# Kernel tuning notes

Hardware: AMD Instinct MI355X
Metric: run time of the kernel (lower is better)

## Reference

```python
import jax, jax.numpy as jnp
import numpy as np

N_NODES = 100000
N_EDGES = 600000
D = 128
BN_EPS = 1e-5


def _segment_mean(msgs, seg_ids, num_segments):
    # sum messages per destination node, divide by in-degree (0-deg nodes -> 0)
    s = jax.ops.segment_sum(msgs, seg_ids, num_segments=num_segments)
    cnt = jax.ops.segment_sum(jnp.ones((msgs.shape[0],), msgs.dtype), seg_ids,
                              num_segments=num_segments)
    return s / jnp.maximum(cnt, 1.0)[:, None]


def setup_inputs() -> dict:
    key = jax.random.key(0)
    ks = jax.random.split(key, 8)
    sc = 1.0 / np.sqrt(D)
    return {
        "node_embs": jax.random.normal(ks[0], (N_NODES, D), jnp.float32),
        "edge_embs": jax.random.normal(ks[1], (N_EDGES, D), jnp.float32),
        "W_O": jax.random.normal(ks[2], (D, D), jnp.float32) * sc,
        "b_O": jnp.zeros((D,), jnp.float32),
        "W_I": jax.random.normal(ks[3], (D, D), jnp.float32) * sc,
        "b_I": jnp.zeros((D,), jnp.float32),
        "W_S": jax.random.normal(ks[4], (D, D), jnp.float32) * sc,
        "b_S": jnp.zeros((D,), jnp.float32),
        "gamma": jnp.ones((D,), jnp.float32),
        "beta": jnp.zeros((D,), jnp.float32),
        "src": jax.random.randint(ks[5], (N_EDGES,), 0, N_NODES),
        "dst": jax.random.randint(ks[6], (N_EDGES,), 0, N_NODES),
    }


def reference(node_embs, edge_embs, W_O, b_O, W_I, b_I, W_S, b_S, gamma, beta, src, dst):
    N = node_embs.shape[0]
    # comp_opt == 'TransE': message = u_sub_e = h_src - h_edge
    # original graph: aggregate at dst -> ho
    ho = _segment_mean(node_embs[src] - edge_embs, dst, N)
    # reverse graph: edges flipped, aggregate at original src -> hi
    hi = _segment_mean(node_embs[dst] - edge_embs, src, N)
    # dropout is identity in eval; combine three projections (weights are [out,in])
    h = ((ho @ W_O.T + b_O) + (hi @ W_I.T + b_I) + (node_embs @ W_S.T + b_S)) / 3.0
    # BatchNorm1d with batch statistics (training-mode normalization, biased var)
    mu = jnp.mean(h, axis=0)
    var = jnp.mean((h - mu) ** 2, axis=0)
    h = (h - mu) * jax.lax.rsqrt(var + BN_EPS) * gamma + beta
    return h
```

## Files before the change

kernel.cpp:

```cpp
#include <hip/hip_runtime.h>
#include <hip/hip_bf16.h>

#define NN 100000
#define NE 600000
#define DD 128
#define NBLK 98

typedef __attribute__((ext_vector_type(8))) short short8_t;
typedef __attribute__((ext_vector_type(4))) float float4_t;

__device__ __forceinline__ unsigned short f2bf(float f) {
    union { float f; unsigned int i; } v; v.f = f;
    unsigned int r = v.i + 0x7fffu + ((v.i >> 16) & 1u);
    return (unsigned short)(r >> 16);
}


__global__ __launch_bounds__(256) void k_hist(
    const int* __restrict__ src, const int* __restrict__ dst,
    int* __restrict__ cnt_o, int* __restrict__ cnt_i)
{
    int e = blockIdx.x * 256 + threadIdx.x;
    if (e < NE) {
        atomicAdd(&cnt_o[dst[e]], 1);
        atomicAdd(&cnt_i[src[e]], 1);
    }
}

__global__ __launch_bounds__(256) void k_scanA(
    const int* __restrict__ cnt_o, const int* __restrict__ cnt_i,
    int* __restrict__ ptr_o, int* __restrict__ ptr_i, int* __restrict__ bsum)
{
    __shared__ int sh[256];
    const int* cnt = blockIdx.y ? cnt_i : cnt_o;
    int* ptr       = blockIdx.y ? ptr_i : ptr_o;
    int t = threadIdx.x;
    int base = blockIdx.x * 1024 + t * 4;
    int c[4];
    #pragma unroll
    for (int j = 0; j < 4; j++) c[j] = (base + j < NN) ? cnt[base + j] : 0;
    int s = c[0] + c[1] + c[2] + c[3];
    sh[t] = s;
    __syncthreads();
    for (int off = 1; off < 256; off <<= 1) {
        int v = (t >= off) ? sh[t - off] : 0;
        __syncthreads();
        sh[t] += v;
        __syncthreads();
    }
    int excl = sh[t] - s;
    int e0 = excl, e1 = e0 + c[0], e2 = e1 + c[1], e3 = e2 + c[2];
    if (base     < NN) ptr[base]     = e0;
    if (base + 1 < NN) ptr[base + 1] = e1;
    if (base + 2 < NN) ptr[base + 2] = e2;
    if (base + 3 < NN) ptr[base + 3] = e3;
    if (t == 255) bsum[blockIdx.y * 128 + blockIdx.x] = sh[255];
}

__global__ __launch_bounds__(128) void k_scanB(int* __restrict__ bsum)
{
    __shared__ int sh[128];
    int t = threadIdx.x;
    int* b = bsum + blockIdx.y * 128;
    int v = (t < NBLK) ? b[t] : 0;
    sh[t] = v;
    __syncthreads();
    for (int off = 1; off < 128; off <<= 1) {
        int u = (t >= off) ? sh[t - off] : 0;
        __syncthreads();
        sh[t] += u;
        __syncthreads();
    }
    b[t] = sh[t] - v;
}

__global__ __launch_bounds__(256) void k_scanC(
    int* __restrict__ ptr_o, int* __restrict__ ptr_i, const int* __restrict__ bsum)
{
    int* ptr = blockIdx.y ? ptr_i : ptr_o;
    int off = bsum[blockIdx.y * 128 + blockIdx.x];
    int base = blockIdx.x * 1024 + threadIdx.x * 4;
    #pragma unroll
    for (int j = 0; j < 4; j++)
        if (base + j < NN) ptr[base + j] += off;
    if (blockIdx.x == 0 && threadIdx.x == 0) ptr[NN] = NE;
}

__global__ __launch_bounds__(256) void k_fill(
    const int* __restrict__ src, const int* __restrict__ dst,
    const int* __restrict__ ptr_o, const int* __restrict__ ptr_i,
    int* __restrict__ cur_o, int* __restrict__ cur_i,
    int2* __restrict__ list_o, int2* __restrict__ list_i)
{
    int e = blockIdx.x * 256 + threadIdx.x;
    if (e < NE) {
        int s = src[e], t = dst[e];
        int p = atomicAdd(&cur_o[t], 1);
        list_o[ptr_o[t] + p] = make_int2(e, s);
        int q = atomicAdd(&cur_i[s], 1);
        list_i[ptr_i[s] + q] = make_int2(e, t);
    }
}

__global__ __launch_bounds__(256) void k_gather(
    const float* __restrict__ node, const float* __restrict__ edge,
    const int* __restrict__ ptr_o, const int* __restrict__ ptr_i,
    const int2* __restrict__ list_o, const int2* __restrict__ list_i,
    float* __restrict__ acc_o, float* __restrict__ acc_i)
{
    int gid = blockIdx.x * 4 + (threadIdx.x >> 6);
    int l = threadIdx.x & 63;
    int half = l >> 5;
    int li = l & 31;
    int dirI = gid >= NN;
    int n = gid - (dirI ? NN : 0);
    const int* ptr   = dirI ? ptr_i  : ptr_o;
    const int2* list = dirI ? list_i : list_o;
    float* acc       = dirI ? acc_i  : acc_o;

    int p0 = ptr[n], p1 = ptr[n + 1];
    int deg = p1 - p0;
    int degc = (deg < 64) ? deg : 64;

    int2 eu = make_int2(0, 0);
    if (l < degc) eu = list[p0 + l];

    float4_t a = {0.f, 0.f, 0.f, 0.f};
    for (int t = 0; t < degc; t += 8) {
        int es[4], us[4];
        float ms[4];
        float4_t xs[4], ys[4];
        #pragma unroll
        for (int b = 0; b < 4; b++) {
            int i0 = t + 2 * b;
            int l0 = (i0     < 64) ? i0     : 0;
            int l1 = (i0 + 1 < 64) ? i0 + 1 : 0;
            int e0 = __builtin_amdgcn_readlane(eu.x, l0);
            int u0 = __builtin_amdgcn_readlane(eu.y, l0);
            int e1 = __builtin_amdgcn_readlane(eu.x, l1);
            int u1 = __builtin_amdgcn_readlane(eu.y, l1);
            es[b] = half ? e1 : e0;
            us[b] = half ? u1 : u0;
            ms[b] = (i0 + half < degc) ? 1.0f : 0.0f;
        }
        #pragma unroll
        for (int b = 0; b < 4; b++) {
            xs[b] = *((const float4_t*)(node + (size_t)us[b] * DD) + li);
            ys[b] = *((const float4_t*)(edge + (size_t)es[b] * DD) + li);
        }
        #pragma unroll
        for (int b = 0; b < 4; b++) {
            #pragma unroll
            for (int c = 0; c < 4; c++)
                a[c] = fmaf(xs[b][c] - ys[b][c], ms[b], a[c]);
        }
    }
    for (int j = p0 + 64 + half; j < p1; j += 2) {
        int2 t = list[j];
        float4_t x = *((const float4_t*)(node + (size_t)t.y * DD) + li);
        float4_t y = *((const float4_t*)(edge + (size_t)t.x * DD) + li);
        a += x - y;
    }

    float4_t b;
    #pragma unroll
    for (int c = 0; c < 4; c++) b[c] = __shfl_xor(a[c], 32);
    a += b;

    float inv = (deg > 0) ? 1.0f / (float)deg : 0.0f;
    a *= inv;
    if (half == 0)
        *((float4_t*)(acc + (size_t)n * DD) + li) = a;
}

__global__ __launch_bounds__(256) void k_gemm(
    const float* acc_o, const float* acc_i,
    const float* __restrict__ node,
    const float* __restrict__ W0, const float* __restrict__ W1, const float* __restrict__ W2,
    const float* __restrict__ b0, const float* __restrict__ b1, const float* __restrict__ b2,
    float* h, float* __restrict__ col_sum, float* __restrict__ col_sumsq)
{
    __shared__ unsigned short s_a[32 * 40];
    __shared__ unsigned short s_b[128 * 40];
    __shared__ float s_red[2 * 4 * 128];

    const int tid = threadIdx.x;
    const int n0 = blockIdx.x * 32;
    const int w  = tid >> 6;
    const int l  = tid & 63;
    const int q  = l >> 4;
    const int li = l & 15;

    float4_t acc[2][2];
    #pragma unroll
    for (int i = 0; i < 2; i++)
        #pragma unroll
        for (int j = 0; j < 2; j++) acc[i][j] = (float4_t){0.f, 0.f, 0.f, 0.f};

    const int srow = tid >> 3;
    const int skq  = tid & 7;

    for (int kc = 0; kc < 12; kc++) {
        const int m  = kc >> 2;
        const int k0 = (kc & 3) * 32;
        const float* X = (m == 0) ? acc_o : (m == 1) ? acc_i : node;
        const float* W = (m == 0) ? W0    : (m == 1) ? W1    : W2;

        __syncthreads();

        {
            float4 v = *(const float4*)&X[(size_t)(n0 + srow) * DD + k0 + 4 * skq];
            ushort4 o = { f2bf(v.x), f2bf(v.y), f2bf(v.z), f2bf(v.w) };
            *(ushort4*)&s_a[srow * 40 + 4 * skq] = o;
        }
        #pragma unroll
        for (int p = 0; p < 4; p++) {
            int row = 32 * p + srow;
            float4 v = *(const float4*)&W[row * DD + k0 + 4 * skq];
            ushort4 o = { f2bf(v.x), f2bf(v.y), f2bf(v.z), f2bf(v.w) };
            *(ushort4*)&s_b[row * 40 + 4 * skq] = o;
        }
        __syncthreads();

        short8_t af0 = *(const short8_t*)&s_a[li * 40 + q * 8];
        short8_t af1 = *(const short8_t*)&s_a[(16 + li) * 40 + q * 8];
        short8_t bf0 = *(const short8_t*)&s_b[(32 * w + li) * 40 + q * 8];
        short8_t bf1 = *(const short8_t*)&s_b[(32 * w + 16 + li) * 40 + q * 8];

        acc[0][0] = __builtin_amdgcn_mfma_f32_16x16x32_bf16(af0, bf0, acc[0][0], 0, 0, 0);
        acc[0][1] = __builtin_amdgcn_mfma_f32_16x16x32_bf16(af0, bf1, acc[0][1], 0, 0, 0);
        acc[1][0] = __builtin_amdgcn_mfma_f32_16x16x32_bf16(af1, bf0, acc[1][0], 0, 0, 0);
        acc[1][1] = __builtin_amdgcn_mfma_f32_16x16x32_bf16(af1, bf1, acc[1][1], 0, 0, 0);
    }

    const float third = 1.0f / 3.0f;
    #pragma unroll
    for (int j = 0; j < 2; j++) {
        int c = 32 * w + 16 * j + li;
        float bsum = b0[c] + b1[c] + b2[c];
        float s = 0.f, sq = 0.f;
        #pragma unroll
        for (int i = 0; i < 2; i++)
            #pragma unroll
            for (int reg = 0; reg < 4; reg++) {
                int r = n0 + 16 * i + q * 4 + reg;
                float v = (acc[i][j][reg] + bsum) * third;
                h[(size_t)r * DD + c] = v;
                s += v; sq += v * v;
            }
        s_red[q * 128 + c]       = s;
        s_red[512 + q * 128 + c] = sq;
    }
    __syncthreads();
    if (tid < 128) {
        float s = 0.f, sq = 0.f;
        #pragma unroll
        for (int r4 = 0; r4 < 4; r4++) {
            s  += s_red[r4 * 128 + tid];
            sq += s_red[512 + r4 * 128 + tid];
        }
        unsafeAtomicAdd(col_sum + tid, s);
        unsafeAtomicAdd(col_sumsq + tid, sq);
    }
}

__global__ void k_stats(const float* __restrict__ col_sum, const float* __restrict__ col_sumsq,
                        const float* __restrict__ gamma, const float* __restrict__ beta,
                        float* __restrict__ sc, float* __restrict__ bs)
{
    int t = threadIdx.x;
    float mu  = col_sum[t]   * (1.0f / NN);
    float var = col_sumsq[t] * (1.0f / NN) - mu * mu;
    var = fmaxf(var, 0.0f);
    float rs = rsqrtf(var + 1e-5f);
    float g = gamma[t];
    sc[t] = rs * g;
    bs[t] = beta[t] - mu * rs * g;
}

__global__ __launch_bounds__(256) void k_norm(const float* __restrict__ h,
        const float* __restrict__ sc, const float* __restrict__ bs,
        float* __restrict__ out)
{
    __shared__ float ssc[128], sbs[128];
    int tid = threadIdx.x;
    if (tid < 128) { ssc[tid] = sc[tid]; sbs[tid] = bs[tid]; }
    __syncthreads();
    size_t base = ((size_t)blockIdx.x * 256 + tid) * 4;
    float4 v = *(const float4*)(h + base);
    int j = (int)(base & 127);
    float4 o;
    o.x = fmaf(v.x, ssc[j],     sbs[j]);
    o.y = fmaf(v.y, ssc[j + 1], sbs[j + 1]);
    o.z = fmaf(v.z, ssc[j + 2], sbs[j + 2]);
    o.w = fmaf(v.w, ssc[j + 3], sbs[j + 3]);
    *(float4*)(out + base) = o;
}

extern "C" void kernel_launch(void* const* d_in, const int* in_sizes, int n_in,
                              void* d_out, int out_size, void* d_ws, size_t ws_size,
                              hipStream_t stream)
{
    const float* node  = (const float*)d_in[0];
    const float* edge  = (const float*)d_in[1];
    const float* W0    = (const float*)d_in[2];
    const float* b0    = (const float*)d_in[3];
    const float* W1    = (const float*)d_in[4];
    const float* b1    = (const float*)d_in[5];
    const float* W2    = (const float*)d_in[6];
    const float* b2    = (const float*)d_in[7];
    const float* gamma = (const float*)d_in[8];
    const float* beta  = (const float*)d_in[9];
    const int* src = (const int*)d_in[10];
    const int* dst = (const int*)d_in[11];
    float* out = (float*)d_out;

    const size_t NB = (size_t)NN * DD;
    float* acc_o = (float*)d_ws;
    float* acc_i = acc_o + NB;
    int* cnt_o = (int*)(acc_i + NB);
    int* cnt_i = cnt_o + NN;
    int* cur_o = cnt_i + NN;
    int* cur_i = cur_o + NN;
    float* col_sum   = (float*)(cur_i + NN);
    float* col_sumsq = col_sum + DD;
    int* ptr_o = (int*)(col_sumsq + DD);
    int* ptr_i = ptr_o + (NN + 1);
    int* bsum  = ptr_i + (NN + 1);
    int2* list_o = (int2*)(bsum + 256);
    int2* list_i = list_o + NE;
    float* sc = (float*)(list_i + NE);
    float* bs = sc + DD;
    float* h  = acc_o;

    size_t zbytes = (size_t)(4 * NN + 2 * DD) * sizeof(int);
    hipMemsetAsync(cnt_o, 0, zbytes, stream);

    int egrid = (NE + 255) / 256;
    k_hist <<<egrid, 256, 0, stream>>>(src, dst, cnt_o, cnt_i);
    k_scanA<<<dim3(NBLK, 2), 256, 0, stream>>>(cnt_o, cnt_i, ptr_o, ptr_i, bsum);
    k_scanB<<<dim3(1, 2), 128, 0, stream>>>(bsum);
    k_scanC<<<dim3(NBLK, 2), 256, 0, stream>>>(ptr_o, ptr_i, bsum);
    k_fill <<<egrid, 256, 0, stream>>>(src, dst, ptr_o, ptr_i, cur_o, cur_i, list_o, list_i);
    k_gather<<<(2 * NN) / 4, 256, 0, stream>>>(node, edge,
                                               ptr_o, ptr_i, list_o, list_i, acc_o, acc_i);
    k_gemm<<<NN / 32, 256, 0, stream>>>(acc_o, acc_i, node,
                                        W0, W1, W2, b0, b1, b2,
                                        h, col_sum, col_sumsq);
    k_stats<<<1, 128, 0, stream>>>(col_sum, col_sumsq, gamma, beta, sc, bs);
    k_norm<<<(NN * DD) / 1024, 256, 0, stream>>>(h, sc, bs, out);
}
```

Measured before the change: 827.1 us.

## Fuse neighbor gather into GEMM kernel with bf16 aggregates kept in LDS

After: 759.2 us. -8.2%, faster.

```diff
diff --git a/kernel.cpp b/kernel.cpp
--- a/kernel.cpp
+++ b/kernel.cpp
@@ -102,94 +102,105 @@
     }
 }
 
-__global__ __launch_bounds__(256) void k_gather(
+__global__ __launch_bounds__(256) void k_gg(
     const float* __restrict__ node, const float* __restrict__ edge,
     const int* __restrict__ ptr_o, const int* __restrict__ ptr_i,
     const int2* __restrict__ list_o, const int2* __restrict__ list_i,
-    float* __restrict__ acc_o, float* __restrict__ acc_i)
-{
-    int gid = blockIdx.x * 4 + (threadIdx.x >> 6);
-    int l = threadIdx.x & 63;
-    int half = l >> 5;
-    int li = l & 31;
-    int dirI = gid >= NN;
-    int n = gid - (dirI ? NN : 0);
-    const int* ptr   = dirI ? ptr_i  : ptr_o;
-    const int2* list = dirI ? list_i : list_o;
-    float* acc       = dirI ? acc_i  : acc_o;
-
-    int p0 = ptr[n], p1 = ptr[n + 1];
-    int deg = p1 - p0;
-    int degc = (deg < 64) ? deg : 64;
-
-    int2 eu = make_int2(0, 0);
-    if (l < degc) eu = list[p0 + l];
-
-    float4_t a = {0.f, 0.f, 0.f, 0.f};
-    for (int t = 0; t < degc; t += 8) {
-        int es[4], us[4];
-        float ms[4];
-        float4_t xs[4], ys[4];
-        #pragma unroll
-        for (int b = 0; b < 4; b++) {
-            int i0 = t + 2 * b;
-            int l0 = (i0     < 64) ? i0     : 0;
-            int l1 = (i0 + 1 < 64) ? i0 + 1 : 0;
-            int e0 = __builtin_amdgcn_readlane(eu.x, l0);
-            int u0 = __builtin_amdgcn_readlane(eu.y, l0);
-            int e1 = __builtin_amdgcn_readlane(eu.x, l1);
-            int u1 = __builtin_amdgcn_readlane(eu.y, l1);
-            es[b] = half ? e1 : e0;
-            us[b] = half ? u1 : u0;
-            ms[b] = (i0 + half < degc) ? 1.0f : 0.0f;
-        }
-        #pragma unroll
-        for (int b = 0; b < 4; b++) {
-            xs[b] = *((const float4_t*)(node + (size_t)us[b] * DD) + li);
-            ys[b] = *((const float4_t*)(edge + (size_t)es[b] * DD) + li);
-        }
-        #pragma unroll
-        for (int b = 0; b < 4; b++) {
-            #pragma unroll
-            for (int c = 0; c < 4; c++)
-                a[c] = fmaf(xs[b][c] - ys[b][c], ms[b], a[c]);
-        }
-    }
-    for (int j = p0 + 64 + half; j < p1; j += 2) {
-        int2 t = list[j];
-        float4_t x = *((const float4_t*)(node + (size_t)t.y * DD) + li);
-        float4_t y = *((const float4_t*)(edge + (size_t)t.x * DD) + li);
-        a += x - y;
-    }
-
-    float4_t b;
-    #pragma unroll
-    for (int c = 0; c < 4; c++) b[c] = __shfl_xor(a[c], 32);
-    a += b;
-
-    float inv = (deg > 0) ? 1.0f / (float)deg : 0.0f;
-    a *= inv;
-    if (half == 0)
-        *((float4_t*)(acc + (size_t)n * DD) + li) = a;
-}
-
-__global__ __launch_bounds__(256) void k_gemm(
-    const float* acc_o, const float* acc_i,
-    const float* __restrict__ node,
     const float* __restrict__ W0, const float* __restrict__ W1, const float* __restrict__ W2,
     const float* __restrict__ b0, const float* __restrict__ b1, const float* __restrict__ b2,
-    float* h, float* __restrict__ col_sum, float* __restrict__ col_sumsq)
-{
-    __shared__ unsigned short s_a[32 * 40];
+    float* __restrict__ h, float* __restrict__ col_sum, float* __restrict__ col_sumsq)
+{
+    __shared__ unsigned short s_x[32 * 392];
     __shared__ unsigned short s_b[128 * 40];
-    __shared__ float s_red[2 * 4 * 128];
+    float* s_red = (float*)s_b;
 
     const int tid = threadIdx.x;
     const int n0 = blockIdx.x * 32;
     const int w  = tid >> 6;
     const int l  = tid & 63;
+    const int half = l >> 5;
+    const int li32 = l & 31;
     const int q  = l >> 4;
     const int li = l & 15;
+    const int srow = tid >> 3;
+    const int skq  = tid & 7;
+
+    #pragma unroll
+    for (int c4 = 0; c4 < 4; c4++) {
+        float4 v = *(const float4*)&node[(size_t)(n0 + srow) * DD + c4 * 32 + 4 * skq];
+        ushort4 o = { f2bf(v.x), f2bf(v.y), f2bf(v.z), f2bf(v.w) };
+        *(ushort4*)&s_x[srow * 392 + 256 + c4 * 32 + 4 * skq] = o;
+    }
+    #pragma unroll
+    for (int p = 0; p < 4; p++) {
+        float4 v = *(const float4*)&W0[(32 * p + srow) * DD + 4 * skq];
+        ushort4 o = { f2bf(v.x), f2bf(v.y), f2bf(v.z), f2bf(v.w) };
+        *(ushort4*)&s_b[(32 * p + srow) * 40 + 4 * skq] = o;
+    }
+
+    for (int it = 0; it < 16; it++) {
+        int tsk = w * 16 + it;
+        int dirI = tsk >= 32;
+        int nl = tsk & 31;
+        int n = n0 + nl;
+        const int* ptr   = dirI ? ptr_i  : ptr_o;
+        const int2* list = dirI ? list_i : list_o;
+
+        int p0 = ptr[n], p1 = ptr[n + 1];
+        int deg = p1 - p0;
+        int degc = (deg < 64) ? deg : 64;
+
+        int2 eu = make_int2(0, 0);
+        if (l < degc) eu = list[p0 + l];
+
+        float4_t a = {0.f, 0.f, 0.f, 0.f};
+        for (int t = 0; t < degc; t += 8) {
+            int es[4], us[4];
+            float ms[4];
+            float4_t xs[4], ys[4];
+            #pragma unroll
+            for (int b = 0; b < 4; b++) {
+                int i0 = t + 2 * b;
+                int l0 = (i0     < 64) ? i0     : 0;
+                int l1 = (i0 + 1 < 64) ? i0 + 1 : 0;
+                int e0 = __builtin_amdgcn_readlane(eu.x, l0);
+                int u0 = __builtin_amdgcn_readlane(eu.y, l0);
+                int e1 = __builtin_amdgcn_readlane(eu.x, l1);
+                int u1 = __builtin_amdgcn_readlane(eu.y, l1);
+                es[b] = half ? e1 : e0;
+                us[b] = half ? u1 : u0;
+                ms[b] = (i0 + half < degc) ? 1.0f : 0.0f;
+            }
+            #pragma unroll
+            for (int b = 0; b < 4; b++) {
+                xs[b] = *((const float4_t*)(node + (size_t)us[b] * DD) + li32);
+                ys[b] = *((const float4_t*)(edge + (size_t)es[b] * DD) + li32);
+            }
+            #pragma unroll
+            for (int b = 0; b < 4; b++) {
+                #pragma unroll
+                for (int c = 0; c < 4; c++)
+                    a[c] = fmaf(xs[b][c] - ys[b][c], ms[b], a[c]);
+            }
+        }
+        for (int j = p0 + 64 + half; j < p1; j += 2) {
+            int2 t2 = list[j];
+            float4_t x = *((const float4_t*)(node + (size_t)t2.y * DD) + li32);
+            float4_t y = *((const float4_t*)(edge + (size_t)t2.x * DD) + li32);
+            a += x - y;
+        }
+        float4_t bsh;
+        #pragma unroll
+        for (int c = 0; c < 4; c++) bsh[c] = __shfl_xor(a[c], 32);
+        a += bsh;
+        float inv = (deg > 0) ? 1.0f / (float)deg : 0.0f;
+        a *= inv;
+        if (half == 0) {
+            ushort4 o = { f2bf(a[0]), f2bf(a[1]), f2bf(a[2]), f2bf(a[3]) };
+            *(ushort4*)&s_x[nl * 392 + dirI * 128 + 4 * li32] = o;
+        }
+    }
+    __syncthreads();
 
     float4_t acc[2][2];
     #pragma unroll
@@ -197,33 +208,18 @@
         #pragma unroll
         for (int j = 0; j < 2; j++) acc[i][j] = (float4_t){0.f, 0.f, 0.f, 0.f};
 
-    const int srow = tid >> 3;
-    const int skq  = tid & 7;
-
+    float4 wv[4];
     for (int kc = 0; kc < 12; kc++) {
-        const int m  = kc >> 2;
-        const int k0 = (kc & 3) * 32;
-        const float* X = (m == 0) ? acc_o : (m == 1) ? acc_i : node;
-        const float* W = (m == 0) ? W0    : (m == 1) ? W1    : W2;
-
-        __syncthreads();
-
-        {
-            float4 v = *(const float4*)&X[(size_t)(n0 + srow) * DD + k0 + 4 * skq];
-            ushort4 o = { f2bf(v.x), f2bf(v.y), f2bf(v.z), f2bf(v.w) };
-            *(ushort4*)&s_a[srow * 40 + 4 * skq] = o;
-        }
-        #pragma unroll
-        for (int p = 0; p < 4; p++) {
-            int row = 32 * p + srow;
-            float4 v = *(const float4*)&W[row * DD + k0 + 4 * skq];
-            ushort4 o = { f2bf(v.x), f2bf(v.y), f2bf(v.z), f2bf(v.w) };
-            *(ushort4*)&s_b[row * 40 + 4 * skq] = o;
-        }
-        __syncthreads();
-
-        short8_t af0 = *(const short8_t*)&s_a[li * 40 + q * 8];
-        short8_t af1 = *(const short8_t*)&s_a[(16 + li) * 40 + q * 8];
+        if (kc < 11) {
+            int kn = kc + 1;
+            const float* W = (kn < 4) ? W0 : (kn < 8) ? W1 : W2;
+            int k0 = (kn & 3) * 32;
+            #pragma unroll
+            for (int p = 0; p < 4; p++)
+                wv[p] = *(const float4*)&W[(32 * p + srow) * DD + k0 + 4 * skq];
+        }
+        short8_t af0 = *(const short8_t*)&s_x[li * 392 + kc * 32 + q * 8];
+        short8_t af1 = *(const short8_t*)&s_x[(16 + li) * 392 + kc * 32 + q * 8];
         short8_t bf0 = *(const short8_t*)&s_b[(32 * w + li) * 40 + q * 8];
         short8_t bf1 = *(const short8_t*)&s_b[(32 * w + 16 + li) * 40 + q * 8];
 
@@ -231,7 +227,18 @@
         acc[0][1] = __builtin_amdgcn_mfma_f32_16x16x32_bf16(af0, bf1, acc[0][1], 0, 0, 0);
         acc[1][0] = __builtin_amdgcn_mfma_f32_16x16x32_bf16(af1, bf0, acc[1][0], 0, 0, 0);
         acc[1][1] = __builtin_amdgcn_mfma_f32_16x16x32_bf16(af1, bf1, acc[1][1], 0, 0, 0);
-    }
+
+        if (kc < 11) {
+            __syncthreads();
+            #pragma unroll
+            for (int p = 0; p < 4; p++) {
+                ushort4 o = { f2bf(wv[p].x), f2bf(wv[p].y), f2bf(wv[p].z), f2bf(wv[p].w) };
+                *(ushort4*)&s_b[(32 * p + srow) * 40 + 4 * skq] = o;
+            }
+            __syncthreads();
+        }
+    }
+    __syncthreads();
 
     const float third = 1.0f / 3.0f;
     #pragma unroll
@@ -316,9 +323,8 @@
     float* out = (float*)d_out;
 
     const size_t NB = (size_t)NN * DD;
-    float* acc_o = (float*)d_ws;
-    float* acc_i = acc_o + NB;
-    int* cnt_o = (int*)(acc_i + NB);
+    float* h = (float*)d_ws;
+    int* cnt_o = (int*)(h + NB);
     int* cnt_i = cnt_o + NN;
     int* cur_o = cnt_i + NN;
     int* cur_i = cur_o + NN;
@@ -331,7 +337,6 @@
     int2* list_i = list_o + NE;
     float* sc = (float*)(list_i + NE);
     float* bs = sc + DD;
-    float* h  = acc_o;
 
     size_t zbytes = (size_t)(4 * NN + 2 * DD) * sizeof(int);
     hipMemsetAsync(cnt_o, 0, zbytes, stream);
@@ -342,9 +347,7 @@
     k_scanB<<<dim3(1, 2), 128, 0, stream>>>(bsum);
     k_scanC<<<dim3(NBLK, 2), 256, 0, stream>>>(ptr_o, ptr_i, bsum);
     k_fill <<<egrid, 256, 0, stream>>>(src, dst, ptr_o, ptr_i, cur_o, cur_i, list_o, list_i);
-    k_gather<<<(2 * NN) / 4, 256, 0, stream>>>(node, edge,
-                                               ptr_o, ptr_i, list_o, list_i, acc_o, acc_i);
-    k_gemm<<<NN / 32, 256, 0, stream>>>(acc_o, acc_i, node,
+    k_gg  <<<NN / 32, 256, 0, stream>>>(node, edge, ptr_o, ptr_i, list_o, list_i,
                                         W0, W1, W2, b0, b1, b2,
                                         h, col_sum, col_sumsq);
     k_stats<<<1, 128, 0, stream>>>(col_sum, col_sumsq, gamma, beta, sc, bs);
```
